# Performance work log

Measured on AMD Instinct MI355X. Metric: run time of the kernel, lower is better.

The kernel has to match this reference:

```python
import jax, jax.numpy as jnp
from jax import lax
import numpy as np

B, T, S, H = 64, 256, 512, 1024  # batch, seq_len, state_size, n_hidden
A, NOUT = 64, 64                 # action_size, n_output
HD = H // 2                      # Dense head width = n_hidden/2


def setup_inputs() -> dict:
    key = jax.random.key(0)
    ks = jax.random.split(key, 10)
    inp = {
        "x": jax.random.normal(ks[0], (B, T, S), dtype=jnp.float32),
        "actions": jax.random.normal(ks[1], (B, A), dtype=jnp.float32),
        "horizon": jax.random.uniform(ks[2], (B, 1), dtype=jnp.float32),
        # LSTM params (Keras gate order i, f, g(cell), o)
        "W_x": jax.random.normal(ks[3], (S, 4 * H), dtype=jnp.float32) * 0.05,
        "W_h": jax.random.normal(ks[4], (H, 4 * H), dtype=jnp.float32) * 0.05,
        "b": jax.random.normal(ks[5], (4 * H,), dtype=jnp.float32) * 0.05,
        # Dense(n_hidden/2, relu)
        "Wd1": jax.random.normal(ks[6], (H, HD), dtype=jnp.float32) * 0.05,
        "bd1": jax.random.normal(ks[7], (HD,), dtype=jnp.float32) * 0.05,
        # output Dense(n_output), input dim = HD + A + 1
        "Wd2": jax.random.normal(ks[8], (HD + A + 1, NOUT), dtype=jnp.float32) * 0.05,
        "bd2": jax.random.normal(ks[9], (NOUT,), dtype=jnp.float32) * 0.05,
    }
    return inp


def _lstm_last_h(x, W_x, W_h, b):
    # Precompute input projection for all timesteps in one big GEMM: [B,T,4H]
    x_proj = jnp.einsum('bts,sg->btg', x, W_x) + b

    def step(carry, xt):
        h, c = carry
        z = xt + h @ W_h                      # [B, 4H]
        i, f, g, o = jnp.split(z, 4, axis=-1)  # Keras gate order i,f,g,o
        i = jax.nn.sigmoid(i)
        f = jax.nn.sigmoid(f)
        g = jnp.tanh(g)
        o = jax.nn.sigmoid(o)
        c = f * c + i * g
        h = o * jnp.tanh(c)
        return (h, c), None

    h0 = jnp.zeros((x.shape[0], W_h.shape[0]), dtype=x.dtype)
    (h, _), _ = lax.scan(step, (h0, h0), jnp.swapaxes(x_proj, 0, 1))
    return h  # final hidden state (return_sequences=False)


def reference(x, actions, horizon, W_x, W_h, b, Wd1, bd1, Wd2, bd2):
    h = _lstm_last_h(x, W_x, W_h, b)                   # [B, H]
    hid = jax.nn.relu(h @ Wd1 + bd1)                   # [B, H/2]
    feat = jnp.concatenate([hid, actions, horizon], 1)  # [B, H/2 + A + 1]
    return feat @ Wd2 + bd2                            # [B, n_output], linear output
```

## Files before the change

### kernel.cpp

```cpp
#include <hip/hip_runtime.h>
#include <stdint.h>

#define NB   64
#define NT   256
#define NS   512
#define NH   1024
#define NG   4096
#define NHD  512
#define NA   64
#define NO   64

typedef float f32x4  __attribute__((ext_vector_type(4)));
typedef short bf16x8 __attribute__((ext_vector_type(8)));
typedef int   i32x4  __attribute__((ext_vector_type(4)));

__device__ __forceinline__ unsigned short f2bf(float f) {
    union { float f; unsigned u; } a; a.f = f;
    unsigned u = a.u;
    return (unsigned short)((u + 0x7fffu + ((u >> 16) & 1u)) >> 16);
}
__device__ __forceinline__ float bf2f(unsigned short h) {
    union { unsigned u; float f; } a; a.u = ((unsigned)h) << 16; return a.f;
}
__device__ __forceinline__ float sigm(float x) {
    return __fdividef(1.0f, 1.0f + __expf(-x));
}
__device__ __forceinline__ float tanh_f(float x) {
    float e = __expf(-2.0f * fabsf(x));
    float r = __fdividef(1.0f - e, 1.0f + e);
    return x >= 0.0f ? r : -r;
}

#define GLD(dst, base, off) \
    asm volatile("global_load_dwordx4 %0, %1, off offset:" #off " sc1" \
                 : "=v"(dst) : "v"(base) : "memory")

#define HKS(WN, ks)                                                              \
    {                                                                            \
        asm volatile("s_waitcnt vmcnt(" #WN ")" : "+v"(q[ks]));                  \
        union { i32x4 i; bf16x8 v; } u0; u0.i = q[ks];                           \
        bf16x8 fh = u0.v;                                                        \
        bf16x8 l0 = whl_lds[w][0][ks][lane];                                     \
        bf16x8 l1 = whl_lds[w][1][ks][lane];                                     \
        bf16x8 l2 = whl_lds[w][2][ks][lane];                                     \
        bf16x8 l3 = whl_lds[w][3][ks][lane];                                     \
        acc[0] = __builtin_amdgcn_mfma_f32_16x16x32_bf16(fh, whh[0][ks], acc[0], 0, 0, 0); \
        acc[1] = __builtin_amdgcn_mfma_f32_16x16x32_bf16(fh, whh[1][ks], acc[1], 0, 0, 0); \
        acc[2] = __builtin_amdgcn_mfma_f32_16x16x32_bf16(fh, whh[2][ks], acc[2], 0, 0, 0); \
        acc[3] = __builtin_amdgcn_mfma_f32_16x16x32_bf16(fh, whh[3][ks], acc[3], 0, 0, 0); \
        acc[0] = __builtin_amdgcn_mfma_f32_16x16x32_bf16(fh, l0, acc[0], 0, 0, 0); \
        acc[1] = __builtin_amdgcn_mfma_f32_16x16x32_bf16(fh, l1, acc[1], 0, 0, 0); \
        acc[2] = __builtin_amdgcn_mfma_f32_16x16x32_bf16(fh, l2, acc[2], 0, 0, 0); \
        acc[3] = __builtin_amdgcn_mfma_f32_16x16x32_bf16(fh, l3, acc[3], 0, 0, 0); \
    }

#define WS_HPK   0
#define WS_HF32  262144
#define WS_HID   524288
#define WS_FLG   655360

__global__ void prologue(unsigned int* __restrict__ hpk32,
                         unsigned int* __restrict__ flg32) {
    int idx = blockIdx.x * blockDim.x + threadIdx.x;
    hpk32[idx] = 0u;
    if (idx < 256) flg32[idx] = 0u;
}

__global__ __launch_bounds__(256, 1) void lstm_persist(
    const float* __restrict__ x, const float* __restrict__ Wx,
    const float* __restrict__ Wh, const float* __restrict__ bias,
    unsigned short* __restrict__ hpack, float* __restrict__ hF32,
    int* __restrict__ flags)
{
    const int g    = blockIdx.x >> 6;
    const int bi   = blockIdx.x & 63;
    const int tid  = threadIdx.x;
    const int w    = tid >> 6;
    const int lane = tid & 63;
    const int lm   = lane & 15;
    const int lq   = lane >> 4;

    __shared__ bf16x8 whl_lds[4][4][8][64];
    __shared__ float zl[4][4][16][17];

    bf16x8 wxh[4][4], wxl[4][4];
    bf16x8 whh[4][8];
    #pragma unroll
    for (int nt = 0; nt < 4; ++nt) {
        const int zc = nt * NH + bi * 16 + lm;
        #pragma unroll
        for (int ks = 0; ks < 4; ++ks)
            #pragma unroll
            for (int j = 0; j < 8; ++j) {
                int k = w * 128 + ks * 32 + lq * 8 + j;
                float v = Wx[(size_t)k * NG + zc];
                unsigned short h = f2bf(v);
                wxh[nt][ks][j] = (short)h;
                wxl[nt][ks][j] = (short)f2bf(v - bf2f(h));
            }
        #pragma unroll
        for (int ks = 0; ks < 8; ++ks) {
            bf16x8 lo;
            #pragma unroll
            for (int j = 0; j < 8; ++j) {
                int k = w * 256 + ks * 32 + lq * 8 + j;
                float v = Wh[(size_t)k * NG + zc];
                unsigned short h = f2bf(v);
                whh[nt][ks][j] = (short)h;
                lo[j] = (short)f2bf(v - bf2f(h));
            }
            whl_lds[w][nt][ks][lane] = lo;
        }
    }

    const int et     = tid & 127;
    const int bloc   = et >> 3;
    const int prc    = et & 7;
    const int gbatch = g * 16 + bloc;
    const int colp   = bi * 16 + prc * 2;
    float bgate[2][4];
    #pragma unroll
    for (int j = 0; j < 2; ++j)
        #pragma unroll
        for (int gt = 0; gt < 4; ++gt)
            bgate[j][gt] = bias[gt * NH + colp + j];
    float c2[2] = {0.0f, 0.0f};

    int* const gflags = flags + g * 64;
    int* const myflag = gflags + bi;
    unsigned int* const hpk32 = reinterpret_cast<unsigned int*>(hpack);

    f32x4 xr[4][2];
    {
        const float* xs = x + (size_t)(g * 16 + lm) * NT * NS + w * 128 + lq * 8;
        #pragma unroll
        for (int ks = 0; ks < 4; ++ks) {
            const f32x4* p = reinterpret_cast<const f32x4*>(xs + ks * 32);
            xr[ks][0] = p[0];
            xr[ks][1] = p[1];
        }
    }

    #pragma unroll 1
    for (int t = 0; t < NT; ++t) {
        if (w == 0) {
            const int* fp = gflags + lane;
            for (;;) {
                int v = __hip_atomic_load(fp, __ATOMIC_RELAXED,
                                          __HIP_MEMORY_SCOPE_AGENT);
                if (__all(v >= t)) break;
                __builtin_amdgcn_s_sleep(1);
            }
        }
        __syncthreads();

        const unsigned short* hb0 = hpack + (size_t)(t & 1) * (NB * NH)
                                  + (size_t)(g * 16 + lm) * NH + w * 256 + lq * 8;
        i32x4 q[8];
        GLD(q[0], hb0, 0);   GLD(q[1], hb0, 64);
        GLD(q[2], hb0, 128); GLD(q[3], hb0, 192);
        GLD(q[4], hb0, 256); GLD(q[5], hb0, 320);
        GLD(q[6], hb0, 384); GLD(q[7], hb0, 448);

        f32x4 acc[4];
        #pragma unroll
        for (int nt = 0; nt < 4; ++nt) {
            acc[nt][0] = 0.f; acc[nt][1] = 0.f;
            acc[nt][2] = 0.f; acc[nt][3] = 0.f;
        }
        #pragma unroll
        for (int ks = 0; ks < 4; ++ks) {
            bf16x8 axh, axl;
            f32x4 vlo = xr[ks][0], vhi = xr[ks][1];
            #pragma unroll
            for (int j = 0; j < 4; ++j) {
                unsigned short h0 = f2bf(vlo[j]);
                axh[j]     = (short)h0;
                axl[j]     = (short)f2bf(vlo[j] - bf2f(h0));
                unsigned short h1 = f2bf(vhi[j]);
                axh[4 + j] = (short)h1;
                axl[4 + j] = (short)f2bf(vhi[j] - bf2f(h1));
            }
            #pragma unroll
            for (int nt = 0; nt < 4; ++nt) {
                acc[nt] = __builtin_amdgcn_mfma_f32_16x16x32_bf16(axh, wxh[nt][ks], acc[nt], 0, 0, 0);
                acc[nt] = __builtin_amdgcn_mfma_f32_16x16x32_bf16(axh, wxl[nt][ks], acc[nt], 0, 0, 0);
                acc[nt] = __builtin_amdgcn_mfma_f32_16x16x32_bf16(axl, wxh[nt][ks], acc[nt], 0, 0, 0);
            }
        }

        HKS(7, 0) HKS(6, 1) HKS(5, 2) HKS(4, 3)
        HKS(3, 4) HKS(2, 5) HKS(1, 6) HKS(0, 7)

        #pragma unroll
        for (int nt = 0; nt < 4; ++nt)
            #pragma unroll
            for (int r = 0; r < 4; ++r)
                zl[w][nt][lq * 4 + r][lm] = acc[nt][r];
        __syncthreads();

        if (tid < 128) {
            float hv[2];
            #pragma unroll
            for (int j = 0; j < 2; ++j) {
                const int n = prc * 2 + j;
                float zg[4];
                #pragma unroll
                for (int gt = 0; gt < 4; ++gt) {
                    zg[gt] = zl[0][gt][bloc][n] + zl[1][gt][bloc][n]
                           + zl[2][gt][bloc][n] + zl[3][gt][bloc][n]
                           + bgate[j][gt];
                }
                float ig = sigm(zg[0]);
                float fg = sigm(zg[1]);
                float gg = tanh_f(zg[2]);
                float og = sigm(zg[3]);
                c2[j] = fg * c2[j] + ig * gg;
                hv[j] = og * tanh_f(c2[j]);
            }
            unsigned pk = (unsigned)f2bf(hv[0]) | ((unsigned)f2bf(hv[1]) << 16);
            const size_t po = (size_t)((t + 1) & 1) * (NB * NH / 2)
                            + (size_t)gbatch * (NH / 2) + bi * 8 + prc;
            __hip_atomic_store(hpk32 + po, pk, __ATOMIC_RELAXED, __HIP_MEMORY_SCOPE_AGENT);
            if (t == NT - 1) {
                hF32[(size_t)gbatch * NH + colp]     = hv[0];
                hF32[(size_t)gbatch * NH + colp + 1] = hv[1];
            }
        }

        __syncthreads();
        if (tid == 0)
            __hip_atomic_store(myflag, t + 1, __ATOMIC_RELAXED, __HIP_MEMORY_SCOPE_AGENT);

        if (t + 1 < NT) {
            const float* xs = x + ((size_t)(g * 16 + lm) * NT + (t + 1)) * NS
                                + w * 128 + lq * 8;
            #pragma unroll
            for (int ks = 0; ks < 4; ++ks) {
                const f32x4* p = reinterpret_cast<const f32x4*>(xs + ks * 32);
                xr[ks][0] = p[0];
                xr[ks][1] = p[1];
            }
        }
    }
}

__global__ __launch_bounds__(512) void head1(
    const float* __restrict__ hF32, const float* __restrict__ Wd1,
    const float* __restrict__ bd1, float* __restrict__ hid)
{
    int b = blockIdx.x;
    int n = threadIdx.x;
    const float* hrow = hF32 + (size_t)b * NH;
    float acc = bd1[n];
    #pragma unroll 8
    for (int k = 0; k < NH; ++k)
        acc += hrow[k] * Wd1[(size_t)k * NHD + n];
    hid[(size_t)b * NHD + n] = fmaxf(acc, 0.0f);
}

__global__ __launch_bounds__(256) void head2(
    const float* __restrict__ hid, const float* __restrict__ act,
    const float* __restrict__ hor, const float* __restrict__ Wd2,
    const float* __restrict__ bd2, float* __restrict__ out)
{
    __shared__ float red[4][64];
    int b  = blockIdx.x;
    int n  = threadIdx.x & 63;
    int ks = threadIdx.x >> 6;
    const float* hrow = hid + (size_t)b * NHD;
    float acc = 0.0f;
    #pragma unroll 4
    for (int k = ks * 128; k < ks * 128 + 128; ++k)
        acc += hrow[k] * Wd2[(size_t)k * NO + n];
    if (ks == 1) {
        const float* arow = act + (size_t)b * NA;
        #pragma unroll 4
        for (int k = 0; k < NA; ++k)
            acc += arow[k] * Wd2[(size_t)(NHD + k) * NO + n];
    }
    if (ks == 2) acc += hor[b] * Wd2[(size_t)576 * NO + n];
    if (ks == 0) acc += bd2[n];
    red[ks][n] = acc;
    __syncthreads();
    if (threadIdx.x < 64)
        out[(size_t)b * NO + n] = red[0][n] + red[1][n] + red[2][n] + red[3][n];
}

extern "C" void kernel_launch(void* const* d_in, const int* in_sizes, int n_in,
                              void* d_out, int out_size, void* d_ws, size_t ws_size,
                              hipStream_t stream)
{
    (void)in_sizes; (void)n_in; (void)out_size; (void)ws_size;
    const float* x    = (const float*)d_in[0];
    const float* act  = (const float*)d_in[1];
    const float* hor  = (const float*)d_in[2];
    const float* Wx   = (const float*)d_in[3];
    const float* Wh   = (const float*)d_in[4];
    const float* bias = (const float*)d_in[5];
    const float* Wd1  = (const float*)d_in[6];
    const float* bd1  = (const float*)d_in[7];
    const float* Wd2  = (const float*)d_in[8];
    const float* bd2  = (const float*)d_in[9];
    float* out = (float*)d_out;

    char* wsb = (char*)d_ws;
    unsigned short* hpk = (unsigned short*)(wsb + WS_HPK);
    float* hF32 = (float*)(wsb + WS_HF32);
    float* hid  = (float*)(wsb + WS_HID);
    int*   flg  = (int*)(wsb + WS_FLG);

    prologue<<<256, 256, 0, stream>>>((unsigned int*)(wsb + WS_HPK),
                                      (unsigned int*)(wsb + WS_FLG));

    lstm_persist<<<dim3(256), dim3(256), 0, stream>>>(x, Wx, Wh, bias,
                                                      hpk, hF32, flg);

    head1<<<64, 512, 0, stream>>>(hF32, Wd1, bd1, hid);
    head2<<<64, 256, 0, stream>>>(hid, act, hor, Wd2, bd2, out);
}
```

Measured before the change: 1.432 ms.

## Relay per-step hidden state through per-XCD leader blocks and local mailboxes

Each block reads its XCC id and elects one leader per (XCD, group) through an atomic counter. Each step, the leader polls the global flags, copies the group's hidden-state slice into an XCD-local mailbox and raises a local flag. The other blocks on that XCD poll that local flag and load h from the mailbox with sc0 loads, so they do not all spin on cross-die flags and fetch from far memory. This adds an extra copy and a second synchronisation hop on the critical path of every step. It also depends on hardware register reads and a spin-count fallback to the global path.

Result: slower. 2.111 ms (+47.4%).

```diff
diff --git a/kernel.cpp b/kernel.cpp
--- a/kernel.cpp
+++ b/kernel.cpp
@@ -33,6 +33,9 @@
 
 #define GLD(dst, base, off) \
     asm volatile("global_load_dwordx4 %0, %1, off offset:" #off " sc1" \
+                 : "=v"(dst) : "v"(base) : "memory")
+#define GLD0(dst, base, off) \
+    asm volatile("global_load_dwordx4 %0, %1, off offset:" #off " sc0" \
                  : "=v"(dst) : "v"(base) : "memory")
 
 #define HKS(WN, ks)                                                              \
@@ -58,19 +61,33 @@
 #define WS_HF32  262144
 #define WS_HID   524288
 #define WS_FLG   655360
+#define WS_ECNT  656384
+#define WS_LFLG  656512
+#define WS_MBOX  660608
+#define WS_NEED  2757760
 
 __global__ void prologue(unsigned int* __restrict__ hpk32,
-                         unsigned int* __restrict__ flg32) {
+                         unsigned int* __restrict__ flg32,
+                         unsigned int* __restrict__ misc32,
+                         unsigned int* __restrict__ mbx32,
+                         int use_relay) {
     int idx = blockIdx.x * blockDim.x + threadIdx.x;
     hpk32[idx] = 0u;
     if (idx < 256) flg32[idx] = 0u;
+    if (use_relay) {
+        if (idx < 1056) misc32[idx] = 0u;
+        #pragma unroll
+        for (int i = 0; i < 8; ++i) mbx32[idx + i * 65536] = 0u;
+    }
 }
 
 __global__ __launch_bounds__(256, 1) void lstm_persist(
     const float* __restrict__ x, const float* __restrict__ Wx,
     const float* __restrict__ Wh, const float* __restrict__ bias,
     unsigned short* __restrict__ hpack, float* __restrict__ hF32,
-    int* __restrict__ flags)
+    int* __restrict__ flags, int* __restrict__ ecnt,
+    int* __restrict__ lflg, unsigned short* __restrict__ mbox,
+    int use_relay)
 {
     const int g    = blockIdx.x >> 6;
     const int bi   = blockIdx.x & 63;
@@ -82,6 +99,26 @@
 
     __shared__ bf16x8 whl_lds[4][4][8][64];
     __shared__ float zl[4][4][16][17];
+    __shared__ int s_role[2];
+    __shared__ int s_fb;
+
+    if (tid == 0) {
+        int xcc = 0, rank = 1;
+        if (use_relay) {
+            asm volatile("s_getreg_b32 %0, hwreg(HW_REG_XCC_ID)" : "=s"(xcc));
+            xcc &= 7;
+            rank = atomicAdd(ecnt + (xcc * 4 + g), 1);
+        }
+        s_role[0] = xcc;
+        s_role[1] = rank;
+    }
+    __syncthreads();
+    const int  xcd      = s_role[0];
+    const bool isLeader = (s_role[1] == 0);
+    bool useLocal       = (use_relay != 0);
+    int* const lfp = lflg + (xcd * 4 + g) * 32;
+    unsigned short* const mb_par0 = mbox + (size_t)((xcd * 2 + 0) * 4 + g) * 16384;
+    unsigned short* const mb_par1 = mbox + (size_t)((xcd * 2 + 1) * 4 + g) * 16384;
 
     bf16x8 wxh[4][4], wxl[4][4];
     bf16x8 whh[4][8];
@@ -143,24 +180,79 @@
 
     #pragma unroll 1
     for (int t = 0; t < NT; ++t) {
-        if (w == 0) {
-            const int* fp = gflags + lane;
-            for (;;) {
-                int v = __hip_atomic_load(fp, __ATOMIC_RELAXED,
-                                          __HIP_MEMORY_SCOPE_AGENT);
-                if (__all(v >= t)) break;
-                __builtin_amdgcn_s_sleep(1);
-            }
-        }
-        __syncthreads();
-
-        const unsigned short* hb0 = hpack + (size_t)(t & 1) * (NB * NH)
-                                  + (size_t)(g * 16 + lm) * NH + w * 256 + lq * 8;
+        const int par = t & 1;
+        unsigned short* const mb = par ? mb_par1 : mb_par0;
+
+        if (isLeader) {
+            if (w == 0) {
+                const int* fp = gflags + lane;
+                for (;;) {
+                    int v = __hip_atomic_load(fp, __ATOMIC_RELAXED,
+                                              __HIP_MEMORY_SCOPE_AGENT);
+                    if (__all(v >= t)) break;
+                    __builtin_amdgcn_s_sleep(1);
+                }
+            }
+            __syncthreads();
+            {
+                const unsigned short* cs = hpack + (size_t)par * (NB * NH)
+                                         + (size_t)g * 16384 + tid * 64;
+                i32x4 c0, c1, c2r, c3, c4, c5, c6, c7;
+                GLD(c0, cs, 0);  GLD(c1, cs, 16); GLD(c2r, cs, 32); GLD(c3, cs, 48);
+                GLD(c4, cs, 64); GLD(c5, cs, 80); GLD(c6, cs, 96);  GLD(c7, cs, 112);
+                asm volatile("s_waitcnt vmcnt(0)" ::: "memory");
+                i32x4* cd = reinterpret_cast<i32x4*>(mb + tid * 64);
+                cd[0] = c0; cd[1] = c1; cd[2] = c2r; cd[3] = c3;
+                cd[4] = c4; cd[5] = c5; cd[6] = c6;  cd[7] = c7;
+                asm volatile("s_waitcnt vmcnt(0)" ::: "memory");
+            }
+            __syncthreads();
+            if (tid == 0) *(volatile int*)lfp = t;
+        } else {
+            if (w == 0) {
+                if (useLocal) {
+                    int spins = 0;
+                    for (;;) {
+                        int v;
+                        asm volatile("global_load_dword %0, %1, off sc0\n\t"
+                                     "s_waitcnt vmcnt(0)"
+                                     : "=v"(v) : "v"(lfp) : "memory");
+                        if (__all(v >= t)) break;
+                        if (++spins > 384) { useLocal = false; break; }
+                        __builtin_amdgcn_s_sleep(1);
+                    }
+                }
+                if (!useLocal) {
+                    const int* fp = gflags + lane;
+                    for (;;) {
+                        int v = __hip_atomic_load(fp, __ATOMIC_RELAXED,
+                                                  __HIP_MEMORY_SCOPE_AGENT);
+                        if (__all(v >= t)) break;
+                        __builtin_amdgcn_s_sleep(1);
+                    }
+                }
+                if (lane == 0) s_fb = useLocal ? 0 : 1;
+            }
+            __syncthreads();
+        }
+
+        int fb = 0;
+        if (!isLeader) fb = s_fb;
         i32x4 q[8];
-        GLD(q[0], hb0, 0);   GLD(q[1], hb0, 64);
-        GLD(q[2], hb0, 128); GLD(q[3], hb0, 192);
-        GLD(q[4], hb0, 256); GLD(q[5], hb0, 320);
-        GLD(q[6], hb0, 384); GLD(q[7], hb0, 448);
+        if (fb) {
+            const unsigned short* hb0 = hpack + (size_t)par * (NB * NH)
+                                      + (size_t)(g * 16 + lm) * NH + w * 256 + lq * 8;
+            GLD(q[0], hb0, 0);   GLD(q[1], hb0, 64);
+            GLD(q[2], hb0, 128); GLD(q[3], hb0, 192);
+            GLD(q[4], hb0, 256); GLD(q[5], hb0, 320);
+            GLD(q[6], hb0, 384); GLD(q[7], hb0, 448);
+        } else {
+            const unsigned short* hb0 = mb + (size_t)lm * NH + w * 256 + lq * 8;
+            GLD0(q[0], hb0, 0);   GLD0(q[1], hb0, 64);
+            GLD0(q[2], hb0, 128); GLD0(q[3], hb0, 192);
+            GLD0(q[4], hb0, 256); GLD0(q[5], hb0, 320);
+            GLD0(q[6], hb0, 384); GLD0(q[7], hb0, 448);
+        }
 
         f32x4 acc[4];
         #pragma unroll
@@ -291,7 +383,7 @@
                               void* d_out, int out_size, void* d_ws, size_t ws_size,
                               hipStream_t stream)
 {
-    (void)in_sizes; (void)n_in; (void)out_size; (void)ws_size;
+    (void)in_sizes; (void)n_in; (void)out_size;
     const float* x    = (const float*)d_in[0];
     const float* act  = (const float*)d_in[1];
     const float* hor  = (const float*)d_in[2];
@@ -305,16 +397,25 @@
     float* out = (float*)d_out;
 
     char* wsb = (char*)d_ws;
-    unsigned short* hpk = (unsigned short*)(wsb + WS_HPK);
+    unsigned short* hpk  = (unsigned short*)(wsb + WS_HPK);
     float* hF32 = (float*)(wsb + WS_HF32);
     float* hid  = (float*)(wsb + WS_HID);
     int*   flg  = (int*)(wsb + WS_FLG);
+    int*   ecn  = (int*)(wsb + WS_ECNT);
+    int*   lfl  = (int*)(wsb + WS_LFLG);
+    unsigned short* mbx = (unsigned short*)(wsb + WS_MBOX);
+
+    const int use_relay = (ws_size >= (size_t)WS_NEED) ? 1 : 0;
 
     prologue<<<256, 256, 0, stream>>>((unsigned int*)(wsb + WS_HPK),
-                                      (unsigned int*)(wsb + WS_FLG));
+                                      (unsigned int*)(wsb + WS_FLG),
+                                      (unsigned int*)(wsb + WS_ECNT),
+                                      (unsigned int*)(wsb + WS_MBOX),
+                                      use_relay);
 
     lstm_persist<<<dim3(256), dim3(256), 0, stream>>>(x, Wx, Wh, bias,
-                                                      hpk, hF32, flg);
+                                                      hpk, hF32, flg,
+                                                      ecn, lfl, mbx, use_relay);
 
     head1<<<64, 512, 0, stream>>>(hF32, Wd1, bd1, hid);
     head2<<<64, 256, 0, stream>>>(hid, act, hor, Wd2, bd2, out);
```
